# Performance work log

Measured on AMD Instinct MI355X. Metric: run time of the kernel, lower is better.

The kernel has to match this reference:

```python
import jax, jax.numpy as jnp
import numpy as np
from jax import lax

# Poincare ball, curvature c = 1.0 (geoopt default for CustomPoincare)
SQRT_C = 1.0
BALL_EPS = 1e-3   # projx margin (geoopt-style)
MIN_NORM = 1e-7
BN_EPS = 1e-5


def _norm(x):
    # norm over channel (last) dim, clamped away from 0
    return jnp.maximum(jnp.linalg.norm(x, axis=-1, keepdims=True), MIN_NORM)


def projx(x):
    # clip points back inside the ball of radius (1-eps)/sqrt(c)
    maxnorm = (1.0 - BALL_EPS) / SQRT_C
    n = _norm(x)
    return x * jnp.minimum(1.0, maxnorm / n)


def expmap0(v):
    # exp map at the origin: tanh(sqrt(c)||v||) * v / (sqrt(c)||v||)
    n = _norm(v)
    return projx(jnp.tanh(SQRT_C * n) * v / (SQRT_C * n))


def logmap0(x):
    # log map at the origin: artanh(sqrt(c)||x||) * x / (sqrt(c)||x||)
    n = _norm(x)
    t = jnp.minimum(SQRT_C * n, 1.0 - 1e-5)
    return jnp.arctanh(t) * x / (SQRT_C * n)


def setup_inputs() -> dict:
    key = jax.random.key(0)
    k0, k1 = jax.random.split(key)
    B, C_in, H, W, C_out = 16, 3, 224, 224, 64
    x = jax.random.normal(k0, (B, C_in, H, W), dtype=jnp.float32)
    # Kaiming-ish init for the 3x3 stem conv, HWIO layout
    fan_in = 3 * 3 * C_in
    conv_w = jax.random.normal(k1, (3, 3, C_in, C_out), dtype=jnp.float32) * np.float32(np.sqrt(2.0 / fan_in))
    conv_b = jnp.zeros((C_out,), dtype=jnp.float32)
    bn_gamma = jnp.ones((C_out,), dtype=jnp.float32)
    bn_beta = jnp.zeros((C_out,), dtype=jnp.float32)
    return {"x": x, "conv_w": conv_w, "conv_b": conv_b,
            "bn_gamma": bn_gamma, "bn_beta": bn_beta}


def reference(x, conv_w, conv_b, bn_gamma, bn_beta):
    # x: [B, C, H, W] -> NHWC (channel-last points on the Poincare ball)
    h = jnp.transpose(x, (0, 2, 3, 1))
    h = projx(h)

    # --- PoincareConv2d: tangent-space 3x3 conv (log0 -> conv+bias -> exp0) ---
    u = logmap0(h)
    u = lax.conv_general_dilated(
        u, conv_w, window_strides=(1, 1), padding="SAME",
        dimension_numbers=("NHWC", "HWIO", "NHWC"))
    u = u + conv_b
    h = expmap0(u)

    # --- PoincareBatchNorm2d: tangent-space BN over (B,H,W) per channel ---
    u = logmap0(h)
    mean = jnp.mean(u, axis=(0, 1, 2), keepdims=True)
    var = jnp.var(u, axis=(0, 1, 2), keepdims=True)
    u = (u - mean) * lax.rsqrt(var + BN_EPS) * bn_gamma + bn_beta
    h = expmap0(u)

    # --- PoincareTangentReLU ---
    h = expmap0(jax.nn.relu(logmap0(h)))
    return h  # [B, H, W, C_out]
```

## Files before the change

kernel.cpp:

```cpp
#include <hip/hip_runtime.h>
#include <math.h>

#define B_ 16
#define H_ 224
#define W_ 224
#define HP_ 226
#define WP_ 226
#define CIN_ 3
#define COUT_ 64
#define NPIX_ (B_ * H_ * W_)
#define NPAD_ (B_ * HP_ * WP_)
#define NBLK_ (NPIX_ / 256)
#define MAXNORM_ 0.999f
#define MINN_ 1e-7f
#define TCL_ (1.0f - 1e-5f)
#define LCLAMP_ 3.8002012f
#define BN_EPS_ 1e-5f
#define NF_ ((float)NPIX_)
#define PADW2_ 36

typedef float v4f __attribute__((ext_vector_type(4)));

struct Acc {
  v4f v0, v1, v2, v3, v4, v5, v6, v7, v8, v9, v10, v11, v12, v13, v14, v15;
};

#define EACH16(X) X(0) X(1) X(2) X(3) X(4) X(5) X(6) X(7) \
                  X(8) X(9) X(10) X(11) X(12) X(13) X(14) X(15)
#define EACH8LO(X) X(0) X(1) X(2) X(3) X(4) X(5) X(6) X(7)
#define EACH8HI(X) X(8) X(9) X(10) X(11) X(12) X(13) X(14) X(15)

__global__ void k0_transform(const float* __restrict__ x, float4* __restrict__ u0p) {
  int idx = blockIdx.x * 256 + threadIdx.x;
  if (idx >= NPAD_) return;
  int b = idx / (HP_ * WP_);
  int r = idx % (HP_ * WP_);
  int yp = r / WP_, xp = r % WP_;
  float4 o = make_float4(0.f, 0.f, 0.f, 0.f);
  if (yp >= 1 && yp <= H_ && xp >= 1 && xp <= W_) {
    const float* xb = x + (size_t)b * (CIN_ * H_ * W_) + (size_t)(yp - 1) * W_ + (xp - 1);
    float v0 = xb[0];
    float v1 = xb[H_ * W_];
    float v2 = xb[2 * H_ * W_];
    float n = sqrtf(fmaf(v0, v0, fmaf(v1, v1, v2 * v2)));
    float ncl = fmaxf(n, MINN_);
    float s = fminf(1.0f, MAXNORM_ / ncl);
    float p0 = v0 * s, p1 = v1 * s, p2 = v2 * s;
    float np_ = fmaxf(sqrtf(fmaf(p0, p0, fmaf(p1, p1, p2 * p2))), MINN_);
    float t = fminf(np_, TCL_);
    float ath = 0.5f * __logf(__fdividef(1.0f + t, 1.0f - t));
    float f = __fdividef(ath, np_);
    o.x = p0 * f; o.y = p1 * f; o.z = p2 * f;
  }
  u0p[idx] = o;
}

__device__ __forceinline__ void conv_clamp(const float4* __restrict__ u0p,
                                           const float* __restrict__ wgt,
                                           const float* __restrict__ bias,
                                           int pix, Acc& a) {
  int b = pix / (H_ * W_);
  int r = pix % (H_ * W_);
  int y = r / W_, x = r % W_;
  const float4* base = u0p + ((size_t)b * HP_ + y) * WP_ + x;
  const v4f* b4 = (const v4f*)bias;
#define INIT(i) a.v##i = b4[i];
  EACH16(INIT)
#undef INIT
#define FMA_X(i) a.v##i += in.x * wp[i];
#define FMA_Y(i) a.v##i += in.y * wp[16 + i];
#define FMA_Z(i) a.v##i += in.z * wp[32 + i];
#define TAP(t) { float4 in = base[((t) / 3) * WP_ + ((t) % 3)];              \
                 const v4f* wp = (const v4f*)(wgt + (t) * 3 * COUT_);        \
                 EACH16(FMA_X) EACH16(FMA_Y) EACH16(FMA_Z) }
  TAP(0) TAP(1) TAP(2) TAP(3) TAP(4) TAP(5) TAP(6) TAP(7) TAP(8)
#undef TAP
#undef FMA_X
#undef FMA_Y
#undef FMA_Z
  v4f s2 = (v4f)0.0f;
#define SQ(i) s2 += a.v##i * a.v##i;
  EACH16(SQ)
#undef SQ
  float n2 = s2.x + s2.y + s2.z + s2.w;
  float n = sqrtf(n2);
  float sc = (n > LCLAMP_) ? (LCLAMP_ / n) : 1.0f;
#define SCL(i) a.v##i *= sc;
  EACH16(SCL)
}

__device__ __forceinline__ v4f vshfl_xor(v4f v, int m) {
  v4f r;
  r.x = __shfl_xor(v.x, m, 64);
  r.y = __shfl_xor(v.y, m, 64);
  r.z = __shfl_xor(v.z, m, 64);
  r.w = __shfl_xor(v.w, m, 64);
  return r;
}

template <bool STORE_T>
__global__ void __launch_bounds__(256, 4)
k1_stats(const float4* __restrict__ u0p, const float* __restrict__ wgt,
         const float* __restrict__ bias, float* __restrict__ tbuf,
         float* __restrict__ partials) {
  int pix = blockIdx.x * 256 + threadIdx.x;
  Acc a;
  conv_clamp(u0p, wgt, bias, pix, a);

  __shared__ __align__(16) float stg[4 * 64 * PADW2_];
  __shared__ float red_s[256], red_q[256];
  int lane = threadIdx.x & 63, wid = threadIdx.x >> 6;
  float* row = stg + (size_t)(wid * 64 + lane) * PADW2_;
  int pr8 = lane >> 3, qi = lane & 7;
  const float* rb = stg + (size_t)wid * 64 * PADW2_ + pr8 * PADW2_ + qi * 4;
  v4f* outw = (v4f*)tbuf + ((size_t)blockIdx.x * 256 + wid * 64) * 16;

#define STGA(i) *(v4f*)(row + 4 * (i)) = a.v##i;
  EACH8LO(STGA)
#undef STGA
  __builtin_amdgcn_wave_barrier();
  v4f sA = (v4f)0.0f, qA = (v4f)0.0f;
#pragma unroll
  for (int j = 0; j < 8; j++) {
    v4f v = *(const v4f*)(rb + j * 8 * PADW2_);
    if (STORE_T) __builtin_nontemporal_store(v, outw + (j * 8 + pr8) * 16 + qi);
    sA += v; qA += v * v;
  }
  sA += vshfl_xor(sA, 8);  qA += vshfl_xor(qA, 8);
  sA += vshfl_xor(sA, 16); qA += vshfl_xor(qA, 16);
  sA += vshfl_xor(sA, 32); qA += vshfl_xor(qA, 32);
  if (lane < 8) {
    *(v4f*)&red_s[wid * 32 + qi * 4] = sA;
    *(v4f*)&red_q[wid * 32 + qi * 4] = qA;
  }
  __builtin_amdgcn_wave_barrier();

#define STGB(i) *(v4f*)(row + 4 * ((i) - 8)) = a.v##i;
  EACH8HI(STGB)
#undef STGB
  __builtin_amdgcn_wave_barrier();
  v4f sB = (v4f)0.0f, qB = (v4f)0.0f;
#pragma unroll
  for (int j = 0; j < 8; j++) {
    v4f v = *(const v4f*)(rb + j * 8 * PADW2_);
    if (STORE_T) __builtin_nontemporal_store(v, outw + (j * 8 + pr8) * 16 + 8 + qi);
    sB += v; qB += v * v;
  }
  sB += vshfl_xor(sB, 8);  qB += vshfl_xor(qB, 8);
  sB += vshfl_xor(sB, 16); qB += vshfl_xor(qB, 16);
  sB += vshfl_xor(sB, 32); qB += vshfl_xor(qB, 32);
  if (lane < 8) {
    *(v4f*)&red_s[128 + wid * 32 + qi * 4] = sB;
    *(v4f*)&red_q[128 + wid * 32 + qi * 4] = qB;
  }
  __syncthreads();
  int tid = threadIdx.x;
  if (tid < 128) {
    int c = tid & 63;
    int base = (c >> 5) * 128 + (c & 31);
    const float* rr = (tid < 64) ? red_s : red_q;
    float tot = rr[base] + rr[base + 32] + rr[base + 64] + rr[base + 96];
    partials[(size_t)blockIdx.x * 128 + tid] = tot;
  }
}

__global__ void k2_finalize(const float* __restrict__ partials, const float* __restrict__ gamma,
                            float* __restrict__ stats) {
  int c = blockIdx.x;
  int t = threadIdx.x;
  float s = 0.f, q = 0.f;
  for (int i = t; i < NBLK_; i += 256) {
    s += partials[(size_t)i * 128 + c];
    q += partials[(size_t)i * 128 + 64 + c];
  }
  __shared__ float ls[256], lq[256];
  ls[t] = s; lq[t] = q;
  __syncthreads();
#pragma unroll
  for (int off = 128; off > 0; off >>= 1) {
    if (t < off) { ls[t] += ls[t + off]; lq[t] += lq[t + off]; }
    __syncthreads();
  }
  if (t == 0) {
    float mean = ls[0] / NF_;
    float msq  = lq[0] / NF_;
    float var = msq - mean * mean;
    stats[c] = mean;
    stats[64 + c] = gamma[c] / sqrtf(var + BN_EPS_);
  }
}

__device__ __forceinline__ void bn_relu_exp_store(Acc& a, const float* __restrict__ stats,
                                                  const float* __restrict__ beta,
                                                  float* __restrict__ out) {
  const v4f* mean4 = (const v4f*)stats;
  const v4f* rg4   = (const v4f*)(stats + 64);
  const v4f* beta4 = (const v4f*)beta;
  v4f s2 = (v4f)0.0f;
#define BN(i) { a.v##i = (a.v##i - mean4[i]) * rg4[i] + beta4[i]; s2 += a.v##i * a.v##i; }
  EACH16(BN)
#undef BN
  float nv2 = s2.x + s2.y + s2.z + s2.w;
  float nv = sqrtf(nv2);
  float sv = (nv > LCLAMP_) ? (LCLAMP_ / nv) : 1.0f;
  v4f z2 = (v4f)0.0f;
#define RELU(i) { v4f r = a.v##i * sv;                                      \
                  r.x = fmaxf(r.x, 0.f); r.y = fmaxf(r.y, 0.f);             \
                  r.z = fmaxf(r.z, 0.f); r.w = fmaxf(r.w, 0.f);             \
                  a.v##i = r; z2 += r * r; }
  EACH16(RELU)
#undef RELU
  float nw2 = z2.x + z2.y + z2.z + z2.w;
  float nw = fmaxf(sqrtf(nw2), MINN_);
  float e2 = __expf(2.0f * nw);
  float th = 1.0f - __fdividef(2.0f, e2 + 1.0f);
  float se = __fdividef(th, nw);
  float clip = fminf(1.0f, MAXNORM_ / fmaxf(th, MINN_));
  float fs = se * clip;

  __shared__ __align__(16) float stg[4 * 64 * PADW2_];
  int lane = threadIdx.x & 63, wid = threadIdx.x >> 6;
  float* row = stg + (size_t)(wid * 64 + lane) * PADW2_;
  int pr8 = lane >> 3, qi = lane & 7;
  const float* rb = stg + (size_t)wid * 64 * PADW2_ + pr8 * PADW2_ + qi * 4;
  v4f* outw = (v4f*)out + ((size_t)blockIdx.x * 256 + wid * 64) * 16;

#define STGA(i) *(v4f*)(row + 4 * (i)) = a.v##i * fs;
  EACH8LO(STGA)
#undef STGA
  __builtin_amdgcn_wave_barrier();
#pragma unroll
  for (int j = 0; j < 8; j++) {
    v4f v = *(const v4f*)(rb + j * 8 * PADW2_);
    __builtin_nontemporal_store(v, outw + (j * 8 + pr8) * 16 + qi);
  }
  __builtin_amdgcn_wave_barrier();
#define STGB(i) *(v4f*)(row + 4 * ((i) - 8)) = a.v##i * fs;
  EACH8HI(STGB)
#undef STGB
  __builtin_amdgcn_wave_barrier();
#pragma unroll
  for (int j = 0; j < 8; j++) {
    v4f v = *(const v4f*)(rb + j * 8 * PADW2_);
    __builtin_nontemporal_store(v, outw + (j * 8 + pr8) * 16 + 8 + qi);
  }
}

__global__ void __launch_bounds__(256, 4)
k3_from_t(const float* __restrict__ tbuf, const float* __restrict__ stats,
          const float* __restrict__ beta, float* __restrict__ out) {
  int pix = blockIdx.x * 256 + threadIdx.x;
  const v4f* tp = (const v4f*)tbuf + (size_t)pix * 16;
  Acc a;
#define LOADT(i) a.v##i = tp[i];
  EACH16(LOADT)
#undef LOADT
  bn_relu_exp_store(a, stats, beta, out);
}

__global__ void __launch_bounds__(256, 4)
k3_fused(const float4* __restrict__ u0p, const float* __restrict__ wgt,
         const float* __restrict__ bias, const float* __restrict__ stats,
         const float* __restrict__ beta, float* __restrict__ out) {
  int pix = blockIdx.x * 256 + threadIdx.x;
  Acc a;
  conv_clamp(u0p, wgt, bias, pix, a);
  bn_relu_exp_store(a, stats, beta, out);
}

extern "C" void kernel_launch(void* const* d_in, const int* in_sizes, int n_in,
                              void* d_out, int out_size, void* d_ws, size_t ws_size,
                              hipStream_t stream) {
  const float* x     = (const float*)d_in[0];
  const float* wgt   = (const float*)d_in[1];
  const float* bias  = (const float*)d_in[2];
  const float* gamma = (const float*)d_in[3];
  const float* beta  = (const float*)d_in[4];
  float* out = (float*)d_out;

  char* ws = (char*)d_ws;
  float4* u0p      = (float4*)ws;
  float*  partials = (float*)(ws + (size_t)NPAD_ * 16);
  float*  stats    = (float*)(ws + (size_t)NPAD_ * 16 + (size_t)NBLK_ * 128 * 4);
  size_t  t_off    = (size_t)NPAD_ * 16 + (size_t)NBLK_ * 128 * 4 + 512;
  float*  tbuf     = (float*)(ws + t_off);
  bool have_t = ws_size >= t_off + (size_t)NPIX_ * COUT_ * 4;

  hipLaunchKernelGGL(k0_transform, dim3((NPAD_ + 255) / 256), dim3(256), 0, stream, x, u0p);
  if (have_t) {
    hipLaunchKernelGGL((k1_stats<true>),  dim3(NBLK_), dim3(256), 0, stream, u0p, wgt, bias, tbuf, partials);
    hipLaunchKernelGGL(k2_finalize,       dim3(64),    dim3(256), 0, stream, partials, gamma, stats);
    hipLaunchKernelGGL(k3_from_t,         dim3(NBLK_), dim3(256), 0, stream, tbuf, stats, beta, out);
  } else {
    hipLaunchKernelGGL((k1_stats<false>), dim3(NBLK_), dim3(256), 0, stream, u0p, wgt, bias, tbuf, partials);
    hipLaunchKernelGGL(k2_finalize,       dim3(64),    dim3(256), 0, stream, partials, gamma, stats);
    hipLaunchKernelGGL(k3_fused,          dim3(NBLK_), dim3(256), 0, stream, u0p, wgt, bias, stats, beta, out);
  }
}
```

Baseline: 366.0 us.

## Split conv into channel halves, drop intermediate buffer, recompute conv in final pass

Removes the 205MB intermediate tensor write/read and always recomputes the 3x3 conv in the final kernel. The conv is computed in two 32-channel halves, with each half staged through LDS, which halves live accumulator registers. The per-pixel clamp and ReLU norm scale factors are passed through shared memory and applied when the staged values are read back. This trades a large amount of HBM traffic for a second conv pass, and the ReLU norm is computed algebraically from the pre-scale values.

```diff
diff --git a/kernel.cpp b/kernel.cpp
--- a/kernel.cpp
+++ b/kernel.cpp
@@ -21,14 +21,11 @@
 
 typedef float v4f __attribute__((ext_vector_type(4)));
 
-struct Acc {
-  v4f v0, v1, v2, v3, v4, v5, v6, v7, v8, v9, v10, v11, v12, v13, v14, v15;
+struct Acc8 {
+  v4f v0, v1, v2, v3, v4, v5, v6, v7;
 };
 
-#define EACH16(X) X(0) X(1) X(2) X(3) X(4) X(5) X(6) X(7) \
-                  X(8) X(9) X(10) X(11) X(12) X(13) X(14) X(15)
-#define EACH8LO(X) X(0) X(1) X(2) X(3) X(4) X(5) X(6) X(7)
-#define EACH8HI(X) X(8) X(9) X(10) X(11) X(12) X(13) X(14) X(15)
+#define EACH8(X) X(0) X(1) X(2) X(3) X(4) X(5) X(6) X(7)
 
 __global__ void k0_transform(const float* __restrict__ x, float4* __restrict__ u0p) {
   int idx = blockIdx.x * 256 + threadIdx.x;
@@ -55,38 +52,30 @@
   u0p[idx] = o;
 }
 
-__device__ __forceinline__ void conv_clamp(const float4* __restrict__ u0p,
-                                           const float* __restrict__ wgt,
-                                           const float* __restrict__ bias,
-                                           int pix, Acc& a) {
+__device__ __forceinline__ void conv_half(const float4* __restrict__ u0p,
+                                          const float* __restrict__ wgt,
+                                          const float* __restrict__ bias,
+                                          int pix, int h, Acc8& a) {
   int b = pix / (H_ * W_);
   int r = pix % (H_ * W_);
   int y = r / W_, x = r % W_;
   const float4* base = u0p + ((size_t)b * HP_ + y) * WP_ + x;
   const v4f* b4 = (const v4f*)bias;
-#define INIT(i) a.v##i = b4[i];
-  EACH16(INIT)
+  int h8 = h * 8;
+#define INIT(i) a.v##i = b4[h8 + i];
+  EACH8(INIT)
 #undef INIT
-#define FMA_X(i) a.v##i += in.x * wp[i];
-#define FMA_Y(i) a.v##i += in.y * wp[16 + i];
-#define FMA_Z(i) a.v##i += in.z * wp[32 + i];
+#define FMA_X(i) a.v##i += in.x * wp[h8 + i];
+#define FMA_Y(i) a.v##i += in.y * wp[16 + h8 + i];
+#define FMA_Z(i) a.v##i += in.z * wp[32 + h8 + i];
 #define TAP(t) { float4 in = base[((t) / 3) * WP_ + ((t) % 3)];              \
                  const v4f* wp = (const v4f*)(wgt + (t) * 3 * COUT_);        \
-                 EACH16(FMA_X) EACH16(FMA_Y) EACH16(FMA_Z) }
+                 EACH8(FMA_X) EACH8(FMA_Y) EACH8(FMA_Z) }
   TAP(0) TAP(1) TAP(2) TAP(3) TAP(4) TAP(5) TAP(6) TAP(7) TAP(8)
 #undef TAP
 #undef FMA_X
 #undef FMA_Y
 #undef FMA_Z
-  v4f s2 = (v4f)0.0f;
-#define SQ(i) s2 += a.v##i * a.v##i;
-  EACH16(SQ)
-#undef SQ
-  float n2 = s2.x + s2.y + s2.z + s2.w;
-  float n = sqrtf(n2);
-  float sc = (n > LCLAMP_) ? (LCLAMP_ / n) : 1.0f;
-#define SCL(i) a.v##i *= sc;
-  EACH16(SCL)
 }
 
 __device__ __forceinline__ v4f vshfl_xor(v4f v, int m) {
@@ -97,33 +86,54 @@
   r.w = __shfl_xor(v.w, m, 64);
   return r;
 }
-
-template <bool STORE_T>
+__device__ __forceinline__ v4f vrelu(v4f v) {
+  v.x = fmaxf(v.x, 0.f); v.y = fmaxf(v.y, 0.f);
+  v.z = fmaxf(v.z, 0.f); v.w = fmaxf(v.w, 0.f);
+  return v;
+}
+__device__ __forceinline__ float hsum(v4f v) { return (v.x + v.y) + (v.z + v.w); }
+
 __global__ void __launch_bounds__(256, 4)
 k1_stats(const float4* __restrict__ u0p, const float* __restrict__ wgt,
-         const float* __restrict__ bias, float* __restrict__ tbuf,
-         float* __restrict__ partials) {
+         const float* __restrict__ bias, float* __restrict__ partials) {
   int pix = blockIdx.x * 256 + threadIdx.x;
-  Acc a;
-  conv_clamp(u0p, wgt, bias, pix, a);
-
   __shared__ __align__(16) float stg[4 * 64 * PADW2_];
+  __shared__ float scl[256];
   __shared__ float red_s[256], red_q[256];
   int lane = threadIdx.x & 63, wid = threadIdx.x >> 6;
   float* row = stg + (size_t)(wid * 64 + lane) * PADW2_;
   int pr8 = lane >> 3, qi = lane & 7;
   const float* rb = stg + (size_t)wid * 64 * PADW2_ + pr8 * PADW2_ + qi * 4;
-  v4f* outw = (v4f*)tbuf + ((size_t)blockIdx.x * 256 + wid * 64) * 16;
-
-#define STGA(i) *(v4f*)(row + 4 * (i)) = a.v##i;
-  EACH8LO(STGA)
-#undef STGA
-  __builtin_amdgcn_wave_barrier();
+  const float* scrow = scl + wid * 64;
+
+  Acc8 a;
+  conv_half(u0p, wgt, bias, pix, 0, a);
+  v4f s2v = (v4f)0.0f;
+#define SQ(i) s2v += a.v##i * a.v##i;
+  EACH8(SQ)
+#undef SQ
+  float s2A = hsum(s2v);
+#define STG(i) *(v4f*)(row + 4 * (i)) = a.v##i;
+  EACH8(STG)
+#undef STG
+  __builtin_amdgcn_wave_barrier();
+
+  conv_half(u0p, wgt, bias, pix, 1, a);
+  s2v = (v4f)0.0f;
+#define SQ(i) s2v += a.v##i * a.v##i;
+  EACH8(SQ)
+#undef SQ
+  float n2 = s2A + hsum(s2v);
+  float n = sqrtf(n2);
+  float sc = (n > LCLAMP_) ? (LCLAMP_ / n) : 1.0f;
+  scl[wid * 64 + lane] = sc;
+  __builtin_amdgcn_wave_barrier();
+
   v4f sA = (v4f)0.0f, qA = (v4f)0.0f;
 #pragma unroll
   for (int j = 0; j < 8; j++) {
-    v4f v = *(const v4f*)(rb + j * 8 * PADW2_);
-    if (STORE_T) __builtin_nontemporal_store(v, outw + (j * 8 + pr8) * 16 + qi);
+    float g = scrow[j * 8 + pr8];
+    v4f v = *(const v4f*)(rb + j * 8 * PADW2_) * g;
     sA += v; qA += v * v;
   }
   sA += vshfl_xor(sA, 8);  qA += vshfl_xor(qA, 8);
@@ -135,15 +145,15 @@
   }
   __builtin_amdgcn_wave_barrier();
 
-#define STGB(i) *(v4f*)(row + 4 * ((i) - 8)) = a.v##i;
-  EACH8HI(STGB)
-#undef STGB
+#define STG(i) *(v4f*)(row + 4 * (i)) = a.v##i;
+  EACH8(STG)
+#undef STG
   __builtin_amdgcn_wave_barrier();
   v4f sB = (v4f)0.0f, qB = (v4f)0.0f;
 #pragma unroll
   for (int j = 0; j < 8; j++) {
-    v4f v = *(const v4f*)(rb + j * 8 * PADW2_);
-    if (STORE_T) __builtin_nontemporal_store(v, outw + (j * 8 + pr8) * 16 + 8 + qi);
+    float g = scrow[j * 8 + pr8];
+    v4f v = *(const v4f*)(rb + j * 8 * PADW2_) * g;
     sB += v; qB += v * v;
   }
   sB += vshfl_xor(sB, 8);  qB += vshfl_xor(qB, 8);
@@ -190,82 +200,73 @@
   }
 }
 
-__device__ __forceinline__ void bn_relu_exp_store(Acc& a, const float* __restrict__ stats,
-                                                  const float* __restrict__ beta,
-                                                  float* __restrict__ out) {
+__global__ void __launch_bounds__(256, 4)
+k3_final(const float4* __restrict__ u0p, const float* __restrict__ wgt,
+         const float* __restrict__ bias, const float* __restrict__ stats,
+         const float* __restrict__ beta, float* __restrict__ out) {
+  int pix = blockIdx.x * 256 + threadIdx.x;
+  __shared__ __align__(16) float stg[4 * 64 * PADW2_];
+  __shared__ float gl[256];
+  int lane = threadIdx.x & 63, wid = threadIdx.x >> 6;
+  float* row = stg + (size_t)(wid * 64 + lane) * PADW2_;
+  int pr8 = lane >> 3, qi = lane & 7;
+  const float* rb = stg + (size_t)wid * 64 * PADW2_ + pr8 * PADW2_ + qi * 4;
+  const float* grow = gl + wid * 64;
+  v4f* outw = (v4f*)out + ((size_t)blockIdx.x * 256 + wid * 64) * 16;
+
   const v4f* mean4 = (const v4f*)stats;
   const v4f* rg4   = (const v4f*)(stats + 64);
   const v4f* beta4 = (const v4f*)beta;
-  v4f s2 = (v4f)0.0f;
-#define BN(i) { a.v##i = (a.v##i - mean4[i]) * rg4[i] + beta4[i]; s2 += a.v##i * a.v##i; }
-  EACH16(BN)
-#undef BN
-  float nv2 = s2.x + s2.y + s2.z + s2.w;
+
+  Acc8 a;
+  conv_half(u0p, wgt, bias, pix, 0, a);
+  v4f s2v = (v4f)0.0f, r2v = (v4f)0.0f;
+#define BNA(i) { a.v##i = (a.v##i - mean4[i]) * rg4[i] + beta4[i];           \
+                 s2v += a.v##i * a.v##i; v4f t_ = vrelu(a.v##i); r2v += t_ * t_; }
+  EACH8(BNA)
+#undef BNA
+  float nv2 = hsum(s2v), r2 = hsum(r2v);
+#define STG(i) *(v4f*)(row + 4 * (i)) = a.v##i;
+  EACH8(STG)
+#undef STG
+  __builtin_amdgcn_wave_barrier();
+
+  conv_half(u0p, wgt, bias, pix, 1, a);
+  s2v = (v4f)0.0f; r2v = (v4f)0.0f;
+#define BNB(i) { a.v##i = (a.v##i - mean4[8 + i]) * rg4[8 + i] + beta4[8 + i]; \
+                 s2v += a.v##i * a.v##i; v4f t_ = vrelu(a.v##i); r2v += t_ * t_; }
+  EACH8(BNB)
+#undef BNB
+  nv2 += hsum(s2v); r2 += hsum(r2v);
   float nv = sqrtf(nv2);
   float sv = (nv > LCLAMP_) ? (LCLAMP_ / nv) : 1.0f;
-  v4f z2 = (v4f)0.0f;
-#define RELU(i) { v4f r = a.v##i * sv;                                      \
-                  r.x = fmaxf(r.x, 0.f); r.y = fmaxf(r.y, 0.f);             \
-                  r.z = fmaxf(r.z, 0.f); r.w = fmaxf(r.w, 0.f);             \
-                  a.v##i = r; z2 += r * r; }
-  EACH16(RELU)
-#undef RELU
-  float nw2 = z2.x + z2.y + z2.z + z2.w;
-  float nw = fmaxf(sqrtf(nw2), MINN_);
+  float nw = fmaxf(sv * sqrtf(r2), MINN_);
   float e2 = __expf(2.0f * nw);
   float th = 1.0f - __fdividef(2.0f, e2 + 1.0f);
   float se = __fdividef(th, nw);
   float clip = fminf(1.0f, MAXNORM_ / fmaxf(th, MINN_));
-  float fs = se * clip;
-
-  __shared__ __align__(16) float stg[4 * 64 * PADW2_];
-  int lane = threadIdx.x & 63, wid = threadIdx.x >> 6;
-  float* row = stg + (size_t)(wid * 64 + lane) * PADW2_;
-  int pr8 = lane >> 3, qi = lane & 7;
-  const float* rb = stg + (size_t)wid * 64 * PADW2_ + pr8 * PADW2_ + qi * 4;
-  v4f* outw = (v4f*)out + ((size_t)blockIdx.x * 256 + wid * 64) * 16;
-
-#define STGA(i) *(v4f*)(row + 4 * (i)) = a.v##i * fs;
-  EACH8LO(STGA)
-#undef STGA
-  __builtin_amdgcn_wave_barrier();
-#pragma unroll
-  for (int j = 0; j < 8; j++) {
-    v4f v = *(const v4f*)(rb + j * 8 * PADW2_);
+  float g = se * clip * sv;
+  gl[wid * 64 + lane] = g;
+  __builtin_amdgcn_wave_barrier();
+
+#pragma unroll
+  for (int j = 0; j < 8; j++) {
+    float gv = grow[j * 8 + pr8];
+    v4f v = vrelu(*(const v4f*)(rb + j * 8 * PADW2_)) * gv;
     __builtin_nontemporal_store(v, outw + (j * 8 + pr8) * 16 + qi);
   }
   __builtin_amdgcn_wave_barrier();
-#define STGB(i) *(v4f*)(row + 4 * ((i) - 8)) = a.v##i * fs;
-  EACH8HI(STGB)
-#undef STGB
-  __builtin_amdgcn_wave_barrier();
-#pragma unroll
-  for (int j = 0; j < 8; j++) {
-    v4f v = *(const v4f*)(rb + j * 8 * PADW2_);
+
+#define STG(i) *(v4f*)(row + 4 * (i)) = a.v##i;
+  EACH8(STG)
+#undef STG
+  __builtin_amdgcn_wave_barrier();
+#pragma unroll
+  for (int j = 0; j < 8; j++) {
+    float gv = grow[j * 8 + pr8];
+    v4f v = vrelu(*(const v4f*)(rb + j * 8 * PADW2_)) * gv;
     __builtin_nontemporal_store(v, outw + (j * 8 + pr8) * 16 + 8 + qi);
   }
-}
-
-__global__ void __launch_bounds__(256, 4)
-k3_from_t(const float* __restrict__ tbuf, const float* __restrict__ stats,
-          const float* __restrict__ beta, float* __restrict__ out) {
-  int pix = blockIdx.x * 256 + threadIdx.x;
-  const v4f* tp = (const v4f*)tbuf + (size_t)pix * 16;
-  Acc a;
-#define LOADT(i) a.v##i = tp[i];
-  EACH16(LOADT)
-#undef LOADT
-  bn_relu_exp_store(a, stats, beta, out);
-}
-
-__global__ void __launch_bounds__(256, 4)
-k3_fused(const float4* __restrict__ u0p, const float* __restrict__ wgt,
-         const float* __restrict__ bias, const float* __restrict__ stats,
-         const float* __restrict__ beta, float* __restrict__ out) {
-  int pix = blockIdx.x * 256 + threadIdx.x;
-  Acc a;
-  conv_clamp(u0p, wgt, bias, pix, a);
-  bn_relu_exp_store(a, stats, beta, out);
 }
 
 extern "C" void kernel_launch(void* const* d_in, const int* in_sizes, int n_in,
@@ -282,18 +283,9 @@
   float4* u0p      = (float4*)ws;
   float*  partials = (float*)(ws + (size_t)NPAD_ * 16);
   float*  stats    = (float*)(ws + (size_t)NPAD_ * 16 + (size_t)NBLK_ * 128 * 4);
-  size_t  t_off    = (size_t)NPAD_ * 16 + (size_t)NBLK_ * 128 * 4 + 512;
-  float*  tbuf     = (float*)(ws + t_off);
-  bool have_t = ws_size >= t_off + (size_t)NPIX_ * COUT_ * 4;
 
   hipLaunchKernelGGL(k0_transform, dim3((NPAD_ + 255) / 256), dim3(256), 0, stream, x, u0p);
-  if (have_t) {
-    hipLaunchKernelGGL((k1_stats<true>),  dim3(NBLK_), dim3(256), 0, stream, u0p, wgt, bias, tbuf, partials);
-    hipLaunchKernelGGL(k2_finalize,       dim3(64),    dim3(256), 0, stream, partials, gamma, stats);
-    hipLaunchKernelGGL(k3_from_t,         dim3(NBLK_), dim3(256), 0, stream, tbuf, stats, beta, out);
-  } else {
-    hipLaunchKernelGGL((k1_stats<false>), dim3(NBLK_), dim3(256), 0, stream, u0p, wgt, bias, tbuf, partials);
-    hipLaunchKernelGGL(k2_finalize,       dim3(64),    dim3(256), 0, stream, partials, gamma, stats);
-    hipLaunchKernelGGL(k3_fused,          dim3(NBLK_), dim3(256), 0, stream, u0p, wgt, bias, stats, beta, out);
-  }
-}
+  hipLaunchKernelGGL(k1_stats,     dim3(NBLK_),               dim3(256), 0, stream, u0p, wgt, bias, partials);
+  hipLaunchKernelGGL(k2_finalize,  dim3(64),                  dim3(256), 0, stream, partials, gamma, stats);
+  hipLaunchKernelGGL(k3_final,     dim3(NBLK_),               dim3(256), 0, stream, u0p, wgt, bias, stats, beta, out);
+}
```

Result: faster. 311.1 us (-15.0%).
